# Kernel tuning notes

Hardware: AMD Instinct MI355X
Metric: run time of the kernel (lower is better)

## Reference

```python
import jax, jax.numpy as jnp
import numpy as np

N_MEL = 80; H = 512; HD = H // 2; R = 2; A = 128; NF = 32; K = 31
EMB = 512; ENC = 512; NSYM = 100


def _lstm_layer(x, lengths, Wih, Whh, b):
    # x: [B,T,D]; masked unidirectional LSTM (packed-sequence semantics:
    # state frozen and output zero past each sequence length).
    B, T, _ = x.shape
    Hh = Whh.shape[1]
    def step(carry, inp):
        h, c = carry
        xt, t = inp
        g = xt @ Wih.T + h @ Whh.T + b
        i, f, gg, o = jnp.split(g, 4, axis=-1)
        c_new = jax.nn.sigmoid(f) * c + jax.nn.sigmoid(i) * jnp.tanh(gg)
        h_new = jax.nn.sigmoid(o) * jnp.tanh(c_new)
        m = (t < lengths)[:, None]
        return (jnp.where(m, h_new, h), jnp.where(m, c_new, c)), jnp.where(m, h_new, 0.0)
    init = (jnp.zeros((B, Hh), x.dtype), jnp.zeros((B, Hh), x.dtype))
    _, ys = jax.lax.scan(step, init, (x.transpose(1, 0, 2), jnp.arange(T)))
    return ys.transpose(1, 0, 2)


def _bilstm(x, lengths, fw, bw):
    # bidirectional masked LSTM: backward dir runs on the sequence reversed
    # within its valid length (pack_padded_sequence semantics).
    T = x.shape[1]
    t = jnp.arange(T)
    idx = jnp.clip(lengths[:, None] - 1 - t[None, :], 0)
    x_rev = jnp.take_along_axis(x, idx[:, :, None], axis=1)
    out_f = _lstm_layer(x, lengths, *fw)
    out_r = _lstm_layer(x_rev, lengths, *bw)
    out_b = jnp.take_along_axis(out_r, idx[:, :, None], axis=1)
    out_b = jnp.where((t[None, :] < lengths[:, None])[:, :, None], out_b, 0.0)
    return jnp.concatenate([out_f, out_b], axis=-1)


def _forward(mel, mel_lengths, decoder_inputs, start_embedding,
             l1f_Wih, l1f_Whh, l1f_b, l1b_Wih, l1b_Whh, l1b_b,
             l2f_Wih, l2f_Whh, l2f_b, l2b_Wih, l2b_Whh, l2b_b,
             dec_Wih, dec_Whh, dec_b,
             q_W, m_W, loc_conv_W, loc_W, v_W,
             ph_W, ph_b, ps_W, ps_b):
    B = mel.shape[0]
    x = mel.transpose(0, 2, 1)                                   # [B,T,80]
    out1 = _bilstm(x, mel_lengths, (l1f_Wih, l1f_Whh, l1f_b), (l1b_Wih, l1b_Whh, l1b_b))
    out1 = out1.reshape(B, -1, H * R)                             # [B,T/R,H*R]
    mem_len = jnp.ceil(mel_lengths.astype(jnp.float32) / R).astype(jnp.int32)
    memory = _bilstm(out1, mem_len, (l2f_Wih, l2f_Whh, l2f_b), (l2b_Wih, l2b_Whh, l2b_b))  # [B,T',H]
    Tm = memory.shape[1]
    pad_mask = jnp.arange(Tm)[None, :] >= mem_len[:, None]        # True where padded
    processed_memory = memory @ m_W.T                             # [B,T',A]

    dec_seq = jnp.concatenate([start_embedding[None], decoder_inputs.transpose(2, 0, 1)], axis=0)  # [T+1,B,EMB]

    pad = (K - 1) // 2

    def dec_step(state, dinp):
        h, c, aw, awc, ctx = state
        cell_in = jnp.concatenate([dinp, ctx], axis=-1)
        g = cell_in @ dec_Wih.T + h @ dec_Whh.T + dec_b
        i, f, gg, o = jnp.split(g, 4, axis=-1)
        c = jax.nn.sigmoid(f) * c + jax.nn.sigmoid(i) * jnp.tanh(gg)
        h = jax.nn.sigmoid(o) * jnp.tanh(c)
        # location-sensitive attention
        aw_cat = jnp.stack([aw, awc], axis=1)                     # [B,2,T']
        loc = jax.lax.conv_general_dilated(aw_cat, loc_conv_W, (1,), [(pad, pad)],
                                           dimension_numbers=('NCH', 'OIH', 'NCH'))
        loc = loc.transpose(0, 2, 1) @ loc_W.T                    # [B,T',A]
        q = (h @ q_W.T)[:, None, :]                               # [B,1,A]
        e = jnp.tanh(q + loc + processed_memory) @ v_W.T          # [B,T',1]
        e = jnp.where(pad_mask, -1e9, e[..., 0])
        aw_new = jax.nn.softmax(e, axis=1)
        ctx_new = jnp.einsum('bt,btd->bd', aw_new, memory)
        awc_new = awc + aw_new
        hid = jax.nn.relu(jnp.concatenate([h, ctx_new], axis=-1) @ ph_W.T + ph_b)
        logit = hid @ ps_W.T + ps_b                               # dropout is identity in eval
        return (h, c, aw_new, awc_new, ctx_new), (hid, logit, aw_new)

    z = jnp.zeros((B, H), mel.dtype)
    init = (z, z, jnp.zeros((B, Tm), mel.dtype), jnp.zeros((B, Tm), mel.dtype), z)
    _, (hiddens, logits, aligns) = jax.lax.scan(dec_step, init, dec_seq)
    return (hiddens.transpose(1, 0, 2), logits.transpose(1, 0, 2), aligns.transpose(1, 0, 2))


def setup_inputs() -> dict:
    key = jax.random.key(0)
    ks = iter(jax.random.split(key, 40))
    B, T, TD = 32, 1600, 160
    s = 0.05
    def w(shape):
        return jax.random.normal(next(ks), shape, jnp.float32) * s
    mel_lengths = jax.random.randint(next(ks), (B,), T // 2, T + 1)
    mel_lengths = mel_lengths.at[0].set(T)
    return {
        'mel': jax.random.normal(next(ks), (B, N_MEL, T), jnp.float32),
        'mel_lengths': mel_lengths,
        'decoder_inputs': jax.random.normal(next(ks), (B, EMB, TD), jnp.float32),
        'start_embedding': jax.random.normal(next(ks), (B, EMB), jnp.float32),
        'l1f_Wih': w((4 * HD, N_MEL)), 'l1f_Whh': w((4 * HD, HD)), 'l1f_b': w((4 * HD,)),
        'l1b_Wih': w((4 * HD, N_MEL)), 'l1b_Whh': w((4 * HD, HD)), 'l1b_b': w((4 * HD,)),
        'l2f_Wih': w((4 * HD, H * R)), 'l2f_Whh': w((4 * HD, HD)), 'l2f_b': w((4 * HD,)),
        'l2b_Wih': w((4 * HD, H * R)), 'l2b_Whh': w((4 * HD, HD)), 'l2b_b': w((4 * HD,)),
        'dec_Wih': w((4 * H, EMB + H)), 'dec_Whh': w((4 * H, H)), 'dec_b': w((4 * H,)),
        'q_W': w((A, H)), 'm_W': w((A, H)), 'loc_conv_W': w((NF, 2, K)),
        'loc_W': w((A, NF)), 'v_W': w((1, A)),
        'ph_W': w((ENC, H + H)), 'ph_b': w((ENC,)),
        'ps_W': w((NSYM + 1, ENC)), 'ps_b': w((NSYM + 1,)),
    }


def reference(mel, mel_lengths, decoder_inputs, start_embedding,
              l1f_Wih, l1f_Whh, l1f_b, l1b_Wih, l1b_Whh, l1b_b,
              l2f_Wih, l2f_Whh, l2f_b, l2b_Wih, l2b_Whh, l2b_b,
              dec_Wih, dec_Whh, dec_b,
              q_W, m_W, loc_conv_W, loc_W, v_W,
              ph_W, ph_b, ps_W, ps_b):
    return _forward(mel, mel_lengths, decoder_inputs, start_embedding,
                    l1f_Wih, l1f_Whh, l1f_b, l1b_Wih, l1b_Whh, l1b_b,
                    l2f_Wih, l2f_Whh, l2f_b, l2b_Wih, l2b_Whh, l2b_b,
                    dec_Wih, dec_Whh, dec_b,
                    q_W, m_W, loc_conv_W, loc_W, v_W,
                    ph_W, ph_b, ps_W, ps_b)
```

## Files before the change

### kernel.cpp

```cpp
#include <hip/hip_runtime.h>
#include <hip/hip_bf16.h>

typedef __hip_bfloat16 bf16;
typedef __attribute__((ext_vector_type(8))) short short8v;
typedef __attribute__((ext_vector_type(4))) float float4v;
#define DEVINL __device__ __forceinline__

DEVINL float bfu2f(unsigned int u){ union{unsigned int u; float f;} c; c.u=u; return c.f; }
DEVINL float b2f(bf16 v){ return __bfloat162float(v); }
DEVINL bf16  f2b(float f){ return __float2bfloat16(f); }
DEVINL float sigf(float x){ return 1.f/(1.f+__expf(-x)); }
DEVINL float tanhfast(float x){
  float t=__expf(-2.f*fabsf(x));
  float r=(1.f-t)/(1.f+t);
  return copysignf(r,x);
}
DEVINL void hilo(float x, short& h, short& l){
  bf16 hb = __float2bfloat16(x);
  bf16 lb = __float2bfloat16(x - __bfloat162float(hb));
  h = *(short*)&hb; l = *(short*)&lb;
}
DEVINL void ld4(const bf16* __restrict__ p, float* d){
  uint2 v = *reinterpret_cast<const uint2*>(p);
  d[0]=bfu2f(v.x<<16); d[1]=bfu2f(v.x&0xffff0000u);
  d[2]=bfu2f(v.y<<16); d[3]=bfu2f(v.y&0xffff0000u);
}
DEVINL void ld4(const float* __restrict__ p, float* d){
  float4 v = *reinterpret_cast<const float4*>(p);
  d[0]=v.x; d[1]=v.y; d[2]=v.z; d[3]=v.w;
}
DEVINL void st1(bf16* p, float v){ *p = f2b(v); }
DEVINL void st1(float* p, float v){ *p = v; }

__global__ void k_zero_f(float* p, long n){
  long i=(long)blockIdx.x*256+threadIdx.x, st=(long)gridDim.x*256;
  for(;i<n;i+=st) p[i]=0.f;
}
__global__ void k_zero_b(bf16* p, long n){
  long i=(long)blockIdx.x*256+threadIdx.x, st=(long)gridDim.x*256;
  for(;i<n;i+=st) p[i]=f2b(0.f);
}
__global__ void k_xT96b(const float* __restrict__ mel, bf16* __restrict__ xT){
  int i = blockIdx.x*256+threadIdx.x; if(i>=51200*96) return;
  int m = i/96, d = i - m*96; int b = m/1600, t = m - b*1600;
  xT[i] = f2b((d<80)? mel[((size_t)b*80 + d)*1600 + t] : 0.f);
}
__global__ void k_padW96b2(const float* __restrict__ W, bf16* __restrict__ hi,
                           bf16* __restrict__ lo){
  int i = blockIdx.x*256+threadIdx.x; if(i>=1024*96) return;
  int j=i/96, d=i-j*96;
  float x = (d<80)? W[j*80+d] : 0.f;
  short h,l; hilo(x,h,l);
  hi[i]=*(bf16*)&h; lo[i]=*(bf16*)&l;
}
__global__ void k_cvt2(const float* __restrict__ W, bf16* __restrict__ hi,
                       bf16* __restrict__ lo, int n){
  int i=blockIdx.x*256+threadIdx.x; if(i>=n) return;
  short h,l; hilo(W[i], h, l);
  hi[i]=*(bf16*)&h; lo[i]=*(bf16*)&l;
}
__global__ void k_whh_il8(const float* __restrict__ W, bf16* __restrict__ il){
  int i = blockIdx.x*256+threadIdx.x; if(i>=262144) return;
  int kk = i&7; int j = (i>>3)&1023; int kc = i>>13;
  il[i] = f2b(W[j*256 + kc*8 + kk]);
}
__global__ void k_psW(const float* __restrict__ W, const float* __restrict__ bsrc,
                      float* __restrict__ Wp, float* __restrict__ bp){
  int i=blockIdx.x*256+threadIdx.x;
  if(i<128*512){ int n=i/512,k=i-n*512; Wp[i] = (n<101)? W[n*512+k] : 0.f; }
  else if(i<128*512+128){ int n=i-128*512; bp[n]=(n<101)? bsrc[n]:0.f; }
}
__global__ void k_dseqb(const float* __restrict__ start, const float* __restrict__ dec_in,
                        bf16* __restrict__ dseq){
  int i=blockIdx.x*256+threadIdx.x; if(i>=5152*512) return;
  int r=i/512, e=i-r*512; int s=r/32, b=r-s*32;
  dseq[i] = f2b((s==0)? start[b*512+e] : dec_in[(size_t)b*81920 + e*160 + (s-1)]);
}
__global__ void k_wpd(const float* __restrict__ Wih, bf16* __restrict__ hi,
                      bf16* __restrict__ lo){
  int i=blockIdx.x*256+threadIdx.x; if(i>=2048*512) return;
  int j=i>>9, k=i&511;
  short h,l; hilo(Wih[(size_t)j*1024 + k], h, l);
  hi[i]=*(bf16*)&h; lo[i]=*(bf16*)&l;
}
__global__ void k_wdg(const float* __restrict__ Wih, const float* __restrict__ Whh,
                      bf16* __restrict__ hi, bf16* __restrict__ lo){
  int i=blockIdx.x*256+threadIdx.x; if(i>=2048*1024) return;
  int j=i>>10, k=i&1023;
  float x = (k<512)? Wih[(size_t)j*1024 + 512 + k] : Whh[(size_t)j*512 + (k-512)];
  short h,l; hilo(x,h,l);
  hi[i]=*(bf16*)&h; lo[i]=*(bf16*)&l;
}

template<bool RELU, typename TA, typename TCO>
__global__ __launch_bounds__(256) void gemm64(
    const TA* __restrict__ A, int lda, int T, int TC, int t0,
    const int* __restrict__ lens, int lenDiv, int rev,
    const float* __restrict__ W, int ldw,
    const float* __restrict__ bias,
    TCO* __restrict__ C, int ldc, int K)
{
  __shared__ float As[16][64];
  __shared__ float Ws[16][64];
  const int tid = threadIdx.x;
  const int n0 = blockIdx.x*64, m0 = blockIdx.y*64;
  const int tx = tid & 15, ty = tid >> 4;
  const int r = tid >> 2, c4 = (tid & 3) * 4;
  const int m = m0 + r;
  size_t arow;
  if (lens){
    int b = m / TC, tc = m - b*TC, t = t0 + tc;
    if (rev){
      int L = lens[b]; if (lenDiv==2) L=(L+1)>>1;
      t = L-1-t; if (t<0) t=0;
    }
    arow = (size_t)b*T + t;
  } else arow = (size_t)m;
  float acc[4][4] = {{0.f}};
  for (int k0=0; k0<K; k0+=16){
    float av[4];
    ld4(A + arow*lda + k0 + c4, av);
    const float4 wv = *reinterpret_cast<const float4*>(&W[(size_t)(n0+r)*ldw + k0 + c4]);
    As[c4+0][r] = av[0]; As[c4+1][r] = av[1]; As[c4+2][r] = av[2]; As[c4+3][r] = av[3];
    Ws[c4+0][r] = wv.x; Ws[c4+1][r]=wv.y; Ws[c4+2][r]=wv.z; Ws[c4+3][r]=wv.w;
    __syncthreads();
    #pragma unroll
    for(int k=0;k<16;k++){
      const float4 a = *reinterpret_cast<const float4*>(&As[k][ty*4]);
      const float4 w = *reinterpret_cast<const float4*>(&Ws[k][tx*4]);
      acc[0][0] += a.x*w.x; acc[0][1] += a.x*w.y; acc[0][2] += a.x*w.z; acc[0][3] += a.x*w.w;
      acc[1][0] += a.y*w.x; acc[1][1] += a.y*w.y; acc[1][2] += a.y*w.z; acc[1][3] += a.y*w.w;
      acc[2][0] += a.z*w.x; acc[2][1] += a.z*w.y; acc[2][2] += a.z*w.z; acc[2][3] += a.z*w.w;
      acc[3][0] += a.w*w.x; acc[3][1] += a.w*w.y; acc[3][2] += a.w*w.z; acc[3][3] += a.w*w.w;
    }
    __syncthreads();
  }
  #pragma unroll
  for(int i=0;i<4;i++){
    const size_t row = (size_t)m0 + ty*4 + i;
    #pragma unroll
    for(int j=0;j<4;j++){
      const int col = n0 + tx*4 + j;
      float v = acc[i][j] + (bias ? bias[col] : 0.f);
      if (RELU) v = fmaxf(v, 0.f);
      st1(&C[row*ldc + col], v);
    }
  }
}

template<bool RELU, typename TCO>
__global__ __launch_bounds__(256) void gemmM(
    const bf16* __restrict__ A, int lda, int T, int TC, int t0,
    const int* __restrict__ lens, int lenDiv, int rev,
    const short* __restrict__ Whi, const short* __restrict__ Wlo, int ldw,
    const float* __restrict__ bias,
    TCO* __restrict__ C, int ldc, int K)
{
  __shared__ short As[128][40];
  __shared__ short Bs[2][128][40];
  const int tid = threadIdx.x;
  const int lane = tid & 63, wave = tid >> 6;
  const int wm = wave >> 1, wn = wave & 1;
  const int n0 = blockIdx.x*128, m0 = blockIdx.y*128;

  auto arow_of = [&](int m)->size_t{
    if (lens){
      int b = m / TC, tc = m - b*TC, t = t0 + tc;
      if (rev){ int L=lens[b]; if(lenDiv==2) L=(L+1)>>1; t=L-1-t; if(t<0)t=0; }
      return (size_t)b*T + t;
    }
    return (size_t)m;
  };

  float4v acc[4][4];
  #pragma unroll
  for (int i=0;i<4;++i)
    #pragma unroll
    for (int j=0;j<4;++j) acc[i][j] = (float4v){0.f,0.f,0.f,0.f};

  const int ar = tid>>2, akp = (tid&3)*8;
  const size_t arow0 = arow_of(m0 + ar), arow1 = arow_of(m0 + ar + 64);
  const short* Ash = (const short*)A;

  for (int k0=0; k0<K; k0+=32){
    *(short8v*)&As[ar][akp]    = *(const short8v*)(Ash + arow0*lda + k0 + akp);
    *(short8v*)&As[ar+64][akp] = *(const short8v*)(Ash + arow1*lda + k0 + akp);
    *(short8v*)&Bs[0][ar][akp]    = *(const short8v*)(Whi + (size_t)(n0+ar)*ldw + k0 + akp);
    *(short8v*)&Bs[0][ar+64][akp] = *(const short8v*)(Whi + (size_t)(n0+ar+64)*ldw + k0 + akp);
    *(short8v*)&Bs[1][ar][akp]    = *(const short8v*)(Wlo + (size_t)(n0+ar)*ldw + k0 + akp);
    *(short8v*)&Bs[1][ar+64][akp] = *(const short8v*)(Wlo + (size_t)(n0+ar+64)*ldw + k0 + akp);
    __syncthreads();
    const int l15 = lane & 15, kb8 = (lane>>4)*8;
    short8v a0[4], bh[4], bl[4];
    #pragma unroll
    for (int mt=0;mt<4;++mt) a0[mt] = *(const short8v*)&As[wm*64+mt*16+l15][kb8];
    #pragma unroll
    for (int nt=0;nt<4;++nt){
      bh[nt] = *(const short8v*)&Bs[0][wn*64+nt*16+l15][kb8];
      bl[nt] = *(const short8v*)&Bs[1][wn*64+nt*16+l15][kb8];
    }
    #pragma unroll
    for (int mt=0;mt<4;++mt)
      #pragma unroll
      for (int nt=0;nt<4;++nt){
        acc[mt][nt] = __builtin_amdgcn_mfma_f32_16x16x32_bf16(a0[mt], bh[nt], acc[mt][nt], 0,0,0);
        acc[mt][nt] = __builtin_amdgcn_mfma_f32_16x16x32_bf16(a0[mt], bl[nt], acc[mt][nt], 0,0,0);
      }
    __syncthreads();
  }
  const int l15 = lane & 15, rb = (lane>>4)*4;
  #pragma unroll
  for (int mt=0;mt<4;++mt){
    #pragma unroll
    for (int nt=0;nt<4;++nt){
      const int col = n0 + wn*64 + nt*16 + l15;
      const float bv = bias ? bias[col] : 0.f;
      #pragma unroll
      for (int i=0;i<4;++i){
        const size_t row = (size_t)m0 + wm*64 + mt*16 + rb + i;
        float v = acc[mt][nt][i] + bv;
        if (RELU) v = fmaxf(v, 0.f);
        st1(&C[row*ldc + col], v);
      }
    }
  }
}

__global__ __launch_bounds__(1024) void lstm8(
   const bf16* __restrict__ Pf, const bf16* __restrict__ Pb,
   const bf16* __restrict__ Whf, const bf16* __restrict__ Whb,
   const int* __restrict__ lens, int lenDiv, int t0, int TC,
   bf16* __restrict__ out, int T, float* __restrict__ hc)
{
  const int b = blockIdx.x, dir = blockIdx.y, j = threadIdx.x;
  int L = lens[b]; if (lenDiv==2) L = (L+1)>>1;
  const bf16* P  = (dir ? Pb : Pf) + (size_t)b*TC*1024;
  const bf16* wil = (dir ? Whb : Whf) + (size_t)j*8;
  float* hcp = hc + (size_t)(dir*32+b)*512;
  __shared__ float hs[256];
  __shared__ float gs[1024];
  if (j<256) hs[j] = hcp[j];
  float c = (j<256) ? hcp[256+j] : 0.f;
  __syncthreads();
  int tcEnd = L - t0; if (tcEnd > TC) tcEnd = TC;
  for (int tc=0; tc<tcEnd; ++tc){
    float acc = b2f(P[(size_t)tc*1024 + j]);
    #pragma unroll 8
    for (int kc=0; kc<32; ++kc){
      const uint4 wv = *reinterpret_cast<const uint4*>(wil + (size_t)kc*8192);
      const int k = kc*8;
      acc += bfu2f(wv.x<<16)*hs[k]   + bfu2f(wv.x&0xffff0000u)*hs[k+1]
           + bfu2f(wv.y<<16)*hs[k+2] + bfu2f(wv.y&0xffff0000u)*hs[k+3]
           + bfu2f(wv.z<<16)*hs[k+4] + bfu2f(wv.z&0xffff0000u)*hs[k+5]
           + bfu2f(wv.w<<16)*hs[k+6] + bfu2f(wv.w&0xffff0000u)*hs[k+7];
    }
    gs[j] = acc;
    __syncthreads();
    if (j<256){
      const float cn = sigf(gs[256+j])*c + sigf(gs[j])*tanhfast(gs[512+j]);
      const float hn = sigf(gs[768+j])*tanhfast(cn);
      c = cn;
      const int t = t0+tc;
      const int srow = dir ? (L-1-t) : t;
      out[((size_t)b*T + srow)*512 + dir*256 + j] = f2b(hn);
      hs[j] = hn;
    }
    __syncthreads();
  }
  if (j<256){ hcp[j]=hs[j]; hcp[256+j]=c; }
}

__global__ __launch_bounds__(512) void dec_rest(
  const float* __restrict__ g_buf, const bf16* __restrict__ Pd,
  const float* __restrict__ qW,
  const float* __restrict__ convW, const float* __restrict__ locW,
  const float* __restrict__ vW, const float* __restrict__ PM, const bf16* __restrict__ memB,
  const int* __restrict__ lens,
  float* __restrict__ h_state, float* __restrict__ c_state, float* __restrict__ ctx_state,
  float* __restrict__ aw_state, float* __restrict__ awc_state,
  float* __restrict__ hallctx, bf16* __restrict__ abuf, float* __restrict__ outA, int s)
{
  const int b = blockIdx.x, u = threadIdx.x;
  __shared__ float hsh[512], red[512], aw_s[800], q_s[128], v_s[128];
  __shared__ float convW_s[1984], locW_s[4096];
  for (int i=u; i<1984; i+=512) convW_s[i]=convW[i];
  for (int i=u; i<4096; i+=512) locW_s[i]=locW[i];
  if (u<128) v_s[u]=vW[u];
  {
    const bf16* pd = Pd + (size_t)(s*32+b)*2048;
    const float gi = g_buf[b*2048 + u]      + b2f(pd[u]);
    const float gf = g_buf[b*2048+512+u]    + b2f(pd[512+u]);
    const float gg = g_buf[b*2048+1024+u]   + b2f(pd[1024+u]);
    const float go = g_buf[b*2048+1536+u]   + b2f(pd[1536+u]);
    const float cn = sigf(gf)*c_state[b*512+u] + sigf(gi)*tanhfast(gg);
    const float hn = sigf(go)*tanhfast(cn);
    c_state[b*512+u]=cn; h_state[b*512+u]=hn; hsh[u]=hn;
    hallctx[((size_t)(s*32+b))*1024 + u] = hn;
    abuf[b*1024 + 512 + u] = f2b(hn);
  }
  __syncthreads();
  if (u<128){
    const float* wr = qW + u*512;
    float acc=0.f;
    for (int k=0;k<512;k+=4){
      const float4 w = *(const float4*)&wr[k];
      const float4 h = *(const float4*)&hsh[k];
      acc += w.x*h.x + w.y*h.y + w.z*h.z + w.w*h.w;
    }
    q_s[u]=acc;
  }
  __syncthreads();
  const int mlen = (lens[b]+1)>>1;
  float ex0=0.f, ex1=0.f;
  #pragma unroll
  for (int rep=0; rep<2; ++rep){
    const int t = u + rep*512;
    float ex = 0.f;
    if (t < 800 && t < mlen){
      float convf[32];
      #pragma unroll
      for (int f=0;f<32;++f) convf[f]=0.f;
      for (int k=0;k<31;++k){
        const int pos = t-15+k;
        const bool ok = (pos>=0 && pos<800);
        const float a0 = ok ? aw_state[b*800+pos] : 0.f;
        const float a1 = ok ? awc_state[b*800+pos] : 0.f;
        #pragma unroll
        for (int f=0;f<32;++f)
          convf[f] += convW_s[(f*2+0)*31+k]*a0 + convW_s[(f*2+1)*31+k]*a1;
      }
      const float* pm = PM + ((size_t)b*800 + t)*128;
      float e = 0.f;
      for (int a=0;a<128;++a){
        float loc = 0.f;
        #pragma unroll
        for (int f=0;f<32;++f) loc += convf[f]*locW_s[a*32+f];
        e += v_s[a]*tanhfast(q_s[a]+loc+pm[a]);
      }
      ex = __expf(e);
    }
    if (rep==0) ex0=ex; else ex1=ex;
  }
  red[u]=ex0+ex1; __syncthreads();
  for (int st=256; st>0; st>>=1){
    if (u<st) red[u]+=red[u+st];
    __syncthreads();
  }
  const float invZ = 1.f/red[0];
  {
    const float a0 = ex0*invZ;
    aw_s[u]=a0; aw_state[b*800+u]=a0; awc_state[b*800+u]+=a0;
    outA[((size_t)b*161+s)*800+u] = a0;
    const int t1=u+512;
    if (t1<800){
      const float a1 = ex1*invZ;
      aw_s[t1]=a1; aw_state[b*800+t1]=a1; awc_state[b*800+t1]+=a1;
      outA[((size_t)b*161+s)*800+t1] = a1;
    }
  }
  __syncthreads();
  float ctxa = 0.f;
  for (int t2=0;t2<800;++t2)
    ctxa += aw_s[t2]*b2f(memB[((size_t)b*800+t2)*512 + u]);
  ctx_state[b*512+u]=ctxa;
  hallctx[((size_t)(s*32+b))*1024 + 512 + u] = ctxa;
  abuf[b*1024 + u] = f2b(ctxa);
}

__global__ void k_scat_h(const float* __restrict__ hid, float* __restrict__ outH){
  int i=blockIdx.x*256+threadIdx.x; if(i>=5152*512) return;
  int r=i>>9, d=i&511; int s=r>>5, b=r&31;
  outH[((size_t)b*161+s)*512 + d] = hid[i];
}
__global__ void k_scat_l(const float* __restrict__ lg, float* __restrict__ outL){
  int i=blockIdx.x*256+threadIdx.x; if(i>=5152*101) return;
  int r=i/101, n=i-r*101; int s=r>>5, b=r&31;
  outL[((size_t)b*161+s)*101 + n] = lg[r*128+n];
}

extern "C" void kernel_launch(void* const* d_in, const int* in_sizes, int n_in,
                              void* d_out, int out_size, void* d_ws, size_t ws_size,
                              hipStream_t stream)
{
  const float* mel    = (const float*)d_in[0];
  const int*   lens   = (const int*)  d_in[1];
  const float* dec_in = (const float*)d_in[2];
  const float* start  = (const float*)d_in[3];
  const float* l1fWih = (const float*)d_in[4];
  const float* l1fWhh = (const float*)d_in[5];
  const float* l1fb   = (const float*)d_in[6];
  const float* l1bWih = (const float*)d_in[7];
  const float* l1bWhh = (const float*)d_in[8];
  const float* l1bb   = (const float*)d_in[9];
  const float* l2fWih = (const float*)d_in[10];
  const float* l2fWhh = (const float*)d_in[11];
  const float* l2fb   = (const float*)d_in[12];
  const float* l2bWih = (const float*)d_in[13];
  const float* l2bWhh = (const float*)d_in[14];
  const float* l2bb   = (const float*)d_in[15];
  const float* decWih = (const float*)d_in[16];
  const float* decWhh = (const float*)d_in[17];
  const float* decb   = (const float*)d_in[18];
  const float* qW     = (const float*)d_in[19];
  const float* mW     = (const float*)d_in[20];
  const float* convW  = (const float*)d_in[21];
  const float* locW   = (const float*)d_in[22];
  const float* vW     = (const float*)d_in[23];
  const float* phW    = (const float*)d_in[24];
  const float* phb    = (const float*)d_in[25];
  const float* psW    = (const float*)d_in[26];
  const float* psb    = (const float*)d_in[27];
  (void)in_sizes; (void)n_in; (void)out_size; (void)ws_size;

  char* wsp = (char*)d_ws;
  size_t off = 0;
  auto alloc = [&](size_t bytes)->char*{
    char* p = wsp + off; off += (bytes + 255) & ~(size_t)255; return p;
  };

  float* stateF   = (float*)alloc((size_t)100352*4);
  float* h_state  = stateF;
  float* c_state  = stateF + 16384;
  float* ctx_state= stateF + 32768;
  float* aw_state = stateF + 49152;
  float* awc_state= stateF + 74752;
  float* hc_enc   = (float*)alloc((size_t)32768*4);
  float* g_buf    = (float*)alloc((size_t)262144*4);
  bf16*  abuf     = (bf16*)alloc((size_t)131072*2);
  float* psW_p    = (float*)alloc((size_t)65536*4);
  float* psb_p    = (float*)alloc((size_t)128*4);
  bf16*  whh1f    = (bf16*)alloc((size_t)262144*2);
  bf16*  whh1b    = (bf16*)alloc((size_t)262144*2);
  bf16*  whh2f    = (bf16*)alloc((size_t)262144*2);
  bf16*  whh2b    = (bf16*)alloc((size_t)262144*2);
  bf16*  w_m_h    = (bf16*)alloc((size_t)65536*2);
  bf16*  w_m_l    = (bf16*)alloc((size_t)65536*2);
  bf16*  w_l1f_h  = (bf16*)alloc((size_t)98304*2);
  bf16*  w_l1f_l  = (bf16*)alloc((size_t)98304*2);
  bf16*  w_l1b_h  = (bf16*)alloc((size_t)98304*2);
  bf16*  w_l1b_l  = (bf16*)alloc((size_t)98304*2);

  char* R_X = alloc((size_t)10747904);
  bf16*  xTb   = (bf16*)R_X;
  bf16*  w_l2f_h = (bf16*)R_X;
  bf16*  w_l2f_l = (bf16*)(R_X + 2097152);
  bf16*  w_l2b_h = (bf16*)(R_X + 4194304);
  bf16*  w_l2b_l = (bf16*)(R_X + 6291456);
  bf16*  dseqB = (bf16*)R_X;
  bf16*  w_pd_h = (bf16*)(R_X + 5505024);
  bf16*  w_pd_l = (bf16*)(R_X + 7602176);
  float* hid  = (float*)R_X;
  char* R_P = alloc((size_t)26214400);
  bf16* Pchf = (bf16*)R_P;
  bf16* Pchb = (bf16*)(R_P + 10485760);
  bf16* Pd   = (bf16*)R_P;
  float* logitb = (float*)(R_P + 21495808);
  char* R_O = alloc((size_t)52428800);
  bf16*  out1    = (bf16*)R_O;
  float* PM      = (float*)R_O;
  float* hallctx = (float*)(R_O + 13107200);
  bf16*  w_dg_h  = (bf16*)(R_O + 34340864);
  bf16*  w_dg_l  = (bf16*)(R_O + 38535168);
  char* R_M = alloc((size_t)26214400);
  bf16*  memB = (bf16*)R_M;

  float* outF = (float*)d_out;
  float* outH = outF;
  float* outL = outF + 2637824;
  float* outA = outF + 3158176;

  k_zero_f<<<392,256,0,stream>>>(stateF, 100352);
  k_zero_f<<<128,256,0,stream>>>(hc_enc, 32768);
  k_zero_b<<<512,256,0,stream>>>(abuf, 131072);
  k_xT96b<<<19200,256,0,stream>>>(mel, xTb);
  k_padW96b2<<<384,256,0,stream>>>(l1fWih, w_l1f_h, w_l1f_l);
  k_padW96b2<<<384,256,0,stream>>>(l1bWih, w_l1b_h, w_l1b_l);
  k_whh_il8<<<1024,256,0,stream>>>(l1fWhh, whh1f);
  k_whh_il8<<<1024,256,0,stream>>>(l1bWhh, whh1b);
  k_whh_il8<<<1024,256,0,stream>>>(l2fWhh, whh2f);
  k_whh_il8<<<1024,256,0,stream>>>(l2bWhh, whh2b);
  k_cvt2<<<256,256,0,stream>>>(mW, w_m_h, w_m_l, 65536);
  k_psW<<<257,256,0,stream>>>(psW, psb, psW_p, psb_p);
  k_zero_b<<<2048,256,0,stream>>>(out1, 26214400);
  k_zero_b<<<2048,256,0,stream>>>(memB, 13107200);

  for (int c=0;c<10;++c){
    const int t0 = c*160;
    gemmM<false,bf16><<<dim3(8,40),256,0,stream>>>(xTb,96, 1600,160,t0, lens,1,0,
        (const short*)w_l1f_h,(const short*)w_l1f_l,96, l1fb, Pchf,1024, 96);
    gemmM<false,bf16><<<dim3(8,40),256,0,stream>>>(xTb,96, 1600,160,t0, lens,1,1,
        (const short*)w_l1b_h,(const short*)w_l1b_l,96, l1bb, Pchb,1024, 96);
    lstm8<<<dim3(32,2),1024,0,stream>>>(Pchf,Pchb, whh1f,whh1b, lens,1, t0,160, out1, 1600, hc_enc);
  }

  k_cvt2<<<4096,256,0,stream>>>(l2fWih, w_l2f_h, w_l2f_l, 1048576);
  k_cvt2<<<4096,256,0,stream>>>(l2bWih, w_l2b_h, w_l2b_l, 1048576);

  k_zero_f<<<128,256,0,stream>>>(hc_enc, 32768);
  for (int c=0;c<5;++c){
    const int t0 = c*160;
    gemmM<false,bf16><<<dim3(8,40),256,0,stream>>>(out1,1024, 800,160,t0, lens,2,0,
        (const short*)w_l2f_h,(const short*)w_l2f_l,1024, l2fb, Pchf,1024, 1024);
    gemmM<false,bf16><<<dim3(8,40),256,0,stream>>>(out1,1024, 800,160,t0, lens,2,1,
        (const short*)w_l2b_h,(const short*)w_l2b_l,1024, l2bb, Pchb,1024, 1024);
    lstm8<<<dim3(32,2),1024,0,stream>>>(Pchf,Pchb, whh2f,whh2b, lens,2, t0,160, memB, 800, hc_enc);
  }

  gemmM<false,float><<<dim3(1,200),256,0,stream>>>(memB,512, 0,0,0, nullptr,0,0,
      (const short*)w_m_h,(const short*)w_m_l,512, (const float*)nullptr, PM,128, 512);
  k_zero_b<<<2048,256,0,stream>>>(dseqB, 2686976);
  k_dseqb<<<10304,256,0,stream>>>(start, dec_in, dseqB);
  k_wpd<<<4096,256,0,stream>>>(decWih, w_pd_h, w_pd_l);
  gemmM<false,bf16><<<dim3(16,41),256,0,stream>>>(dseqB,512, 0,0,0, nullptr,0,0,
      (const short*)w_pd_h,(const short*)w_pd_l,512, decb, Pd,2048, 512);
  k_zero_f<<<2048,256,0,stream>>>(hallctx, 5308416);
  k_wdg<<<8192,256,0,stream>>>(decWih, decWhh, w_dg_h, w_dg_l);

  for (int s=0; s<161; ++s){
    gemmM<false,float><<<dim3(16,1),256,0,stream>>>(abuf,1024, 0,0,0, nullptr,0,0,
        (const short*)w_dg_h,(const short*)w_dg_l,1024, (const float*)nullptr, g_buf,2048, 1024);
    dec_rest<<<32,512,0,stream>>>(g_buf, Pd, qW, convW, locW, vW, PM, memB, lens,
                                  h_state, c_state, ctx_state, aw_state, awc_state,
                                  hallctx, abuf, outA, s);
  }

  gemm64<true ,float,float><<<dim3(8,81),256,0,stream>>>(hallctx,1024, 0,0,0, nullptr,0,0,
                                                phW,1024, phb, hid,512, 1024);
  gemm64<false,float,float><<<dim3(2,81),256,0,stream>>>(hid,512, 0,0,0, nullptr,0,0,
                                                psW_p,512, psb_p, logitb,128, 512);
  k_scat_h<<<10304,256,0,stream>>>(hid, outH);
  k_scat_l<<<2033,256,0,stream>>>(logitb, outL);
}
```

Measured before the change: 46.15 ms.

## Replace per-step decoder gate GEMM with FP32 matvec kernel and widen attention block

```diff
diff --git a/kernel.cpp b/kernel.cpp
--- a/kernel.cpp
+++ b/kernel.cpp
@@ -81,14 +81,6 @@
   int i=blockIdx.x*256+threadIdx.x; if(i>=2048*512) return;
   int j=i>>9, k=i&511;
   short h,l; hilo(Wih[(size_t)j*1024 + k], h, l);
-  hi[i]=*(bf16*)&h; lo[i]=*(bf16*)&l;
-}
-__global__ void k_wdg(const float* __restrict__ Wih, const float* __restrict__ Whh,
-                      bf16* __restrict__ hi, bf16* __restrict__ lo){
-  int i=blockIdx.x*256+threadIdx.x; if(i>=2048*1024) return;
-  int j=i>>10, k=i&1023;
-  float x = (k<512)? Wih[(size_t)j*1024 + 512 + k] : Whh[(size_t)j*512 + (k-512)];
-  short h,l; hilo(x,h,l);
   hi[i]=*(bf16*)&h; lo[i]=*(bf16*)&l;
 }
 
@@ -270,33 +262,53 @@
   if (j<256){ hcp[j]=hs[j]; hcp[256+j]=c; }
 }
 
-__global__ __launch_bounds__(512) void dec_rest(
-  const float* __restrict__ g_buf, const bf16* __restrict__ Pd,
-  const float* __restrict__ qW,
+__global__ __launch_bounds__(256) void dec_g(
+  const bf16* __restrict__ Pd, const float* __restrict__ Wih,
+  const float* __restrict__ Whh, const float* __restrict__ h_state,
+  const float* __restrict__ ctx_state, float* __restrict__ g_buf, int s)
+{
+  const int b = blockIdx.x, jt = blockIdx.y, tid = threadIdx.x;
+  const int j = jt*256 + tid;
+  __shared__ float cs[512], hs[512];
+  cs[tid] = ctx_state[b*512+tid]; cs[256+tid] = ctx_state[b*512+256+tid];
+  hs[tid] = h_state[b*512+tid];   hs[256+tid] = h_state[b*512+256+tid];
+  __syncthreads();
+  float acc = b2f(Pd[((size_t)(s*32+b))*2048 + j]);
+  const float* wc = Wih + (size_t)j*1024 + 512;
+  const float* wh = Whh + (size_t)j*512;
+  for (int k=0;k<512;k+=4){
+    const float4 cv = *(const float4*)&cs[k];
+    const float4 hv = *(const float4*)&hs[k];
+    const float4 a  = *(const float4*)&wc[k];
+    const float4 b4 = *(const float4*)&wh[k];
+    acc += a.x*cv.x + a.y*cv.y + a.z*cv.z + a.w*cv.w;
+    acc += b4.x*hv.x + b4.y*hv.y + b4.z*hv.z + b4.w*hv.w;
+  }
+  g_buf[b*2048 + j] = acc;
+}
+
+__global__ __launch_bounds__(1024) void dec_rest(
+  const float* __restrict__ g_buf, const float* __restrict__ qW,
   const float* __restrict__ convW, const float* __restrict__ locW,
   const float* __restrict__ vW, const float* __restrict__ PM, const bf16* __restrict__ memB,
   const int* __restrict__ lens,
   float* __restrict__ h_state, float* __restrict__ c_state, float* __restrict__ ctx_state,
   float* __restrict__ aw_state, float* __restrict__ awc_state,
-  float* __restrict__ hallctx, bf16* __restrict__ abuf, float* __restrict__ outA, int s)
+  float* __restrict__ hallctx, float* __restrict__ outA, int s)
 {
   const int b = blockIdx.x, u = threadIdx.x;
-  __shared__ float hsh[512], red[512], aw_s[800], q_s[128], v_s[128];
+  __shared__ float hsh[512], red[1024], aw_s[800], q_s[128], v_s[128];
   __shared__ float convW_s[1984], locW_s[4096];
-  for (int i=u; i<1984; i+=512) convW_s[i]=convW[i];
-  for (int i=u; i<4096; i+=512) locW_s[i]=locW[i];
+  for (int i=u; i<1984; i+=1024) convW_s[i]=convW[i];
+  for (int i=u; i<4096; i+=1024) locW_s[i]=locW[i];
   if (u<128) v_s[u]=vW[u];
-  {
-    const bf16* pd = Pd + (size_t)(s*32+b)*2048;
-    const float gi = g_buf[b*2048 + u]      + b2f(pd[u]);
-    const float gf = g_buf[b*2048+512+u]    + b2f(pd[512+u]);
-    const float gg = g_buf[b*2048+1024+u]   + b2f(pd[1024+u]);
-    const float go = g_buf[b*2048+1536+u]   + b2f(pd[1536+u]);
+  if (u<512){
+    const float gi = g_buf[b*2048 + u],     gf = g_buf[b*2048+512+u];
+    const float gg = g_buf[b*2048+1024+u],  go = g_buf[b*2048+1536+u];
     const float cn = sigf(gf)*c_state[b*512+u] + sigf(gi)*tanhfast(gg);
     const float hn = sigf(go)*tanhfast(cn);
     c_state[b*512+u]=cn; h_state[b*512+u]=hn; hsh[u]=hn;
     hallctx[((size_t)(s*32+b))*1024 + u] = hn;
-    abuf[b*1024 + 512 + u] = f2b(hn);
   }
   __syncthreads();
   if (u<128){
@@ -311,60 +323,57 @@
   }
   __syncthreads();
   const int mlen = (lens[b]+1)>>1;
-  float ex0=0.f, ex1=0.f;
-  #pragma unroll
-  for (int rep=0; rep<2; ++rep){
-    const int t = u + rep*512;
-    float ex = 0.f;
-    if (t < 800 && t < mlen){
-      float convf[32];
+  const int t = u;
+  float ex = 0.f;
+  if (t < 800 && t < mlen){
+    float convf[32];
+    #pragma unroll
+    for (int f=0;f<32;++f) convf[f]=0.f;
+    for (int k=0;k<31;++k){
+      const int pos = t-15+k;
+      const bool ok = (pos>=0 && pos<800);
+      const float a0 = ok ? aw_state[b*800+pos] : 0.f;
+      const float a1 = ok ? awc_state[b*800+pos] : 0.f;
       #pragma unroll
-      for (int f=0;f<32;++f) convf[f]=0.f;
-      for (int k=0;k<31;++k){
-        const int pos = t-15+k;
-        const bool ok = (pos>=0 && pos<800);
-        const float a0 = ok ? aw_state[b*800+pos] : 0.f;
-        const float a1 = ok ? awc_state[b*800+pos] : 0.f;
-        #pragma unroll
-        for (int f=0;f<32;++f)
-          convf[f] += convW_s[(f*2+0)*31+k]*a0 + convW_s[(f*2+1)*31+k]*a1;
-      }
-      const float* pm = PM + ((size_t)b*800 + t)*128;
-      float e = 0.f;
-      for (int a=0;a<128;++a){
-        float loc = 0.f;
-        #pragma unroll
-        for (int f=0;f<32;++f) loc += convf[f]*locW_s[a*32+f];
-        e += v_s[a]*tanhfast(q_s[a]+loc+pm[a]);
-      }
-      ex = __expf(e);
-    }
-    if (rep==0) ex0=ex; else ex1=ex;
-  }
-  red[u]=ex0+ex1; __syncthreads();
-  for (int st=256; st>0; st>>=1){
+      for (int f=0;f<32;++f)
+        convf[f] += convW_s[(f*2+0)*31+k]*a0 + convW_s[(f*2+1)*31+k]*a1;
+    }
+    const float* pm = PM + ((size_t)b*800 + t)*128;
+    float e = 0.f;
+    for (int a=0;a<128;++a){
+      float loc = 0.f;
+      #pragma unroll
+      for (int f=0;f<32;++f) loc += convf[f]*locW_s[a*32+f];
+      e += v_s[a]*tanhfast(q_s[a]+loc+pm[a]);
+    }
+    ex = __expf(e);
+  }
+  red[u]=ex; __syncthreads();
+  for (int st=512; st>0; st>>=1){
     if (u<st) red[u]+=red[u+st];
     __syncthreads();
   }
   const float invZ = 1.f/red[0];
+  if (t<800){
+    const float a0 = ex*invZ;
+    aw_s[t]=a0; aw_state[b*800+t]=a0; awc_state[b*800+t]+=a0;
+    outA[((size_t)b*161+s)*800+t] = a0;
+  }
+  __syncthreads();
   {
-    const float a0 = ex0*invZ;
-    aw_s[u]=a0; aw_state[b*800+u]=a0; awc_state[b*800+u]+=a0;
-    outA[((size_t)b*161+s)*800+u] = a0;
-    const int t1=u+512;
-    if (t1<800){
-      const float a1 = ex1*invZ;
-      aw_s[t1]=a1; aw_state[b*800+t1]=a1; awc_state[b*800+t1]+=a1;
-      outA[((size_t)b*161+s)*800+t1] = a1;
-    }
+    const int half = u>>9, d = u&511;
+    float acc=0.f;
+    const int tb = half*400;
+    for (int t2=tb; t2<tb+400; ++t2)
+      acc += aw_s[t2]*b2f(memB[((size_t)b*800+t2)*512 + d]);
+    red[half*512 + d] = acc;
   }
   __syncthreads();
-  float ctxa = 0.f;
-  for (int t2=0;t2<800;++t2)
-    ctxa += aw_s[t2]*b2f(memB[((size_t)b*800+t2)*512 + u]);
-  ctx_state[b*512+u]=ctxa;
-  hallctx[((size_t)(s*32+b))*1024 + 512 + u] = ctxa;
-  abuf[b*1024 + u] = f2b(ctxa);
+  if (u<512){
+    const float v = red[u] + red[512+u];
+    ctx_state[b*512+u]=v;
+    hallctx[((size_t)(s*32+b))*1024 + 512 + u] = v;
+  }
 }
 
 __global__ void k_scat_h(const float* __restrict__ hid, float* __restrict__ outH){
@@ -425,8 +434,7 @@
   float* aw_state = stateF + 49152;
   float* awc_state= stateF + 74752;
   float* hc_enc   = (float*)alloc((size_t)32768*4);
-  float* g_buf    = (float*)alloc((size_t)262144*4);
-  bf16*  abuf     = (bf16*)alloc((size_t)131072*2);
+  float* g_buf    = (float*)alloc((size_t)65536*4);
   float* psW_p    = (float*)alloc((size_t)65536*4);
   float* psb_p    = (float*)alloc((size_t)128*4);
   bf16*  whh1f    = (bf16*)alloc((size_t)262144*2);
@@ -459,8 +467,6 @@
   bf16*  out1    = (bf16*)R_O;
   float* PM      = (float*)R_O;
   float* hallctx = (float*)(R_O + 13107200);
-  bf16*  w_dg_h  = (bf16*)(R_O + 34340864);
-  bf16*  w_dg_l  = (bf16*)(R_O + 38535168);
   char* R_M = alloc((size_t)26214400);
   bf16*  memB = (bf16*)R_M;
 
@@ -471,7 +477,6 @@
 
   k_zero_f<<<392,256,0,stream>>>(stateF, 100352);
   k_zero_f<<<128,256,0,stream>>>(hc_enc, 32768);
-  k_zero_b<<<512,256,0,stream>>>(abuf, 131072);
   k_xT96b<<<19200,256,0,stream>>>(mel, xTb);
   k_padW96b2<<<384,256,0,stream>>>(l1fWih, w_l1f_h, w_l1f_l);
   k_padW96b2<<<384,256,0,stream>>>(l1bWih, w_l1b_h, w_l1b_l);
@@ -514,14 +519,12 @@
   gemmM<false,bf16><<<dim3(16,41),256,0,stream>>>(dseqB,512, 0,0,0, nullptr,0,0,
       (const short*)w_pd_h,(const short*)w_pd_l,512, decb, Pd,2048, 512);
   k_zero_f<<<2048,256,0,stream>>>(hallctx, 5308416);
-  k_wdg<<<8192,256,0,stream>>>(decWih, decWhh, w_dg_h, w_dg_l);
 
   for (int s=0; s<161; ++s){
-    gemmM<false,float><<<dim3(16,1),256,0,stream>>>(abuf,1024, 0,0,0, nullptr,0,0,
-        (const short*)w_dg_h,(const short*)w_dg_l,1024, (const float*)nullptr, g_buf,2048, 1024);
-    dec_rest<<<32,512,0,stream>>>(g_buf, Pd, qW, convW, locW, vW, PM, memB, lens,
-                                  h_state, c_state, ctx_state, aw_state, awc_state,
-                                  hallctx, abuf, outA, s);
+    dec_g<<<dim3(32,8),256,0,stream>>>(Pd, decWih, decWhh, h_state, ctx_state, g_buf, s);
+    dec_rest<<<32,1024,0,stream>>>(g_buf, qW, convW, locW, vW, PM, memB, lens,
+                                   h_state, c_state, ctx_state, aw_state, awc_state,
+                                   hallctx, outA, s);
   }
 
   gemm64<true ,float,float><<<dim3(8,81),256,0,stream>>>(hallctx,1024, 0,0,0, nullptr,0,0,
```

Result: faster. 37.95 ms (median of 2 runs) (-17.8%).
